# Optimization experiments

Hardware: AMD Instinct MI355X
Metric: run time of the kernel (lower is better)

## Reference

```python
import jax, jax.numpy as jnp
import numpy as np

N_ITEMS = 50000
N_USERS = 20000
N_NODES = N_ITEMS + N_USERS
D = 128
N_REL = 3
NNZ = 800000
K_LAYERS = 2
B, S, L = 256, 4, 50


def setup_inputs() -> dict:
    key = jax.random.key(0)
    ks = iter(jax.random.split(key, 40))
    stdv = float(1.0 / np.sqrt(D))

    def uni(shape):
        return jax.random.uniform(next(ks), shape, jnp.float32, -stdv, stdv)

    id_emb = (jax.random.normal(next(ks), (N_ITEMS, D), jnp.float32) * 0.1).at[0].set(0.0)  # padding_idx=0
    user_emb = jax.random.normal(next(ks), (N_USERS, D), jnp.float32) * 0.1
    inp = dict(
        id_emb=id_emb, user_emb=user_emb,
        lin_r_w=uni((K_LAYERS, N_REL, D, D)),
        upi_w=uni((K_LAYERS, D, D)), upi_b=uni((K_LAYERS, D)),
        upu_w=uni((K_LAYERS, D, D)), upu_b=uni((K_LAYERS, D)),
        w_ih=uni((3 * D, 2 * D)), w_hh=uni((3 * D, D)),
        b_ih=uni((3 * D,)), b_hh=uni((3 * D,)),
        b_iah=uni((D,)), b_oah=uni((D,)),
        ei_w=uni((D, D)), ei_b=uni((D,)),
        eo_w=uni((D, D)), eo_b=uni((D,)),
        q1_w=uni((D, D)), q2_w=uni((D, D)), att_w=uni((D,)),
        fuse_w=uni((D, 2 * D)), fuse_b=uni((D,)),
    )
    # global heterogeneous graph: COO per relation over item+user nodes
    inp['rel_rows'] = jax.random.randint(next(ks), (N_REL, NNZ), 0, N_NODES, dtype=jnp.int32)
    inp['rel_cols'] = jax.random.randint(next(ks), (N_REL, NNZ), 0, N_NODES, dtype=jnp.int32)
    inp['rel_vals'] = jax.random.uniform(next(ks), (N_REL, NNZ), jnp.float32) * 0.1
    # session batch: every session has length in [2, L]
    lens = jax.random.randint(next(ks), (B, S), 2, L + 1)
    raw = jax.random.randint(next(ks), (B, S, L), 1, N_ITEMS)
    inp['ids'] = (raw * (jnp.arange(L)[None, None, :] < lens[:, :, None])).astype(jnp.int32)
    inp['uid'] = jax.random.randint(next(ks), (B,), 0, N_USERS, dtype=jnp.int32)
    inp['u_type'] = jax.random.randint(next(ks), (B,), 0, 3).astype(jnp.float32)
    return inp


def _hgnn(h_item, h_user, rel_rows, rel_cols, rel_vals, lin_r_w, upi_w, upi_b, upu_w, upu_b):
    Ni = h_item.shape[0]
    N = Ni + h_user.shape[0]
    for k in range(lin_r_w.shape[0]):
        h_all = jnp.concatenate([h_item, h_user], 0)
        msg = jnp.zeros_like(h_all)
        for r in range(rel_rows.shape[0]):
            Wh = h_all @ lin_r_w[k, r].T  # per-relation linear
            msg = msg + jax.ops.segment_sum(Wh[rel_cols[r]] * rel_vals[r][:, None],
                                            rel_rows[r], num_segments=N)  # sparse.mm
        h_item = jax.nn.relu((msg[:Ni] + h_item) @ upi_w[k].T + upi_b[k])
        h_user = jax.nn.relu((msg[Ni:] + h_user) @ upu_w[k].T + upu_b[k])
    return h_item, h_user


def reference(id_emb, user_emb, lin_r_w, upi_w, upi_b, upu_w, upu_b,
              w_ih, w_hh, b_ih, b_hh, b_iah, b_oah,
              ei_w, ei_b, eo_w, eo_b, q1_w, q2_w, att_w, fuse_w, fuse_b,
              rel_rows, rel_cols, rel_vals, ids, uid, u_type):
    Bb, Ss, Ll = ids.shape
    N = Ss * Bb
    ids_sb = jnp.transpose(ids, (1, 0, 2)).reshape(N, Ll)  # session-major, matches torch concat order
    lens = (ids_sb != 0).sum(-1)  # >= 2 by construction -> all sessions valid
    rows = jnp.arange(N)
    target = ids_sb[rows, lens - 1]
    Lp = Ll - 1
    m_in = jnp.arange(Lp)[None, :] < (lens - 1)[:, None]
    seq_in = ids_sb[:, :Lp] * m_in
    # session graph: consecutive-item edges; in-half sub-diagonal, out-half super-diagonal
    valid = (m_in[:, 1:] & m_in[:, :-1]).astype(jnp.float32)  # [N, Lp-1]
    i1 = jnp.arange(1, Lp)
    i0 = jnp.arange(Lp - 1)
    a_in = jnp.zeros((N, Lp, Lp), jnp.float32).at[:, i1, i0].set(valid)
    a_out = jnp.zeros((N, Lp, Lp), jnp.float32).at[:, i0, i1].set(valid)
    deg = jnp.clip(a_in.sum(-1), 1.0, None)[..., None]
    a_in = a_in / deg
    a_out = a_out / deg
    h = id_emb[seq_in]  # [N, Lp, D]
    # SessionGNN GRU-style cell (step=1)
    m_i = jnp.matmul(a_in, h @ ei_w.T + ei_b) + b_iah
    m_o = jnp.matmul(a_out, h @ eo_w.T + eo_b) + b_oah
    gi = jnp.concatenate([m_i, m_o], -1) @ w_ih.T + b_ih
    gh = h @ w_hh.T + b_hh
    i_r, i_i, i_n = jnp.split(gi, 3, -1)
    h_r, h_i, h_n = jnp.split(gh, 3, -1)
    rg = jax.nn.sigmoid(i_r + h_r)
    zg = jax.nn.sigmoid(i_i + h_i)
    ng = jnp.tanh(i_n + rg * h_n)
    h = ng + zg * (h - ng)
    # attention readout
    ht = h[rows, jnp.clip(lens - 2, 0, None)]
    alpha = jax.nn.sigmoid((ht @ q1_w.T)[:, None, :] + h @ q2_w.T) @ att_w  # [N, Lp]
    alpha = alpha * m_in.astype(jnp.float32)
    alpha = alpha / (alpha.sum(1, keepdims=True) + 1e-8)
    c_cur = jnp.einsum('nl,nld->nd', alpha, h)
    # global HGNN user context
    g_item, g_user = _hgnn(id_emb[:N_ITEMS], user_emb[:N_USERS], rel_rows, rel_cols,
                           rel_vals, lin_r_w, upi_w, upi_b, upu_w, upu_b)
    c_hist = g_user[jnp.tile(uid, Ss)]
    reps = jnp.concatenate([c_cur, c_hist], -1) @ fuse_w.T + fuse_b
    return reps, target, jnp.tile(u_type, Ss)
```

## Files before the change

kernel.cpp:

```cpp
#include <hip/hip_runtime.h>
#include <hip/hip_bf16.h>

typedef __hip_bfloat16 bf16;
typedef unsigned int uint32;
typedef __attribute__((ext_vector_type(8))) short short8;
typedef __attribute__((ext_vector_type(4))) float f32x4;
typedef __attribute__((ext_vector_type(2))) float f32x2;
typedef __attribute__((ext_vector_type(4))) uint32 u32x4;

#define N_ITEMS_C 50000
#define N_USERS_C 20000
#define N_NODES_C 70000
#define NNZ_C 800000
#define NSESS 1024
#define LP 49
#define NTOK (NSESS * LP)
#define NBK 137

__device__ __forceinline__ float bflo(uint32 u) { return __uint_as_float(u << 16); }
__device__ __forceinline__ float bfhi(uint32 u) { return __uint_as_float(u & 0xffff0000u); }
__device__ __forceinline__ float bfhi_fast(uint32 u) { return __uint_as_float(u); }
__device__ __forceinline__ uint32 packbf(float a, float b) {
    return (uint32)__bfloat16_as_ushort(__float2bfloat16(a)) |
           ((uint32)__bfloat16_as_ushort(__float2bfloat16(b)) << 16);
}

__global__ void init_hab_kernel(const float2* __restrict__ idp, const float2* __restrict__ usp,
                                uint32* __restrict__ hab) {
    int i = blockIdx.x * 256 + threadIdx.x;
    float2 w = (i < 3200000) ? idp[i] : usp[i - 3200000];
    hab[i] = packbf(w.x, w.y);
}

__global__ __launch_bounds__(256) void bucket_hist_kernel(
    const int* __restrict__ rel_rows, int* __restrict__ bhist)
{
    __shared__ int hist[NBK];
    const int r = blockIdx.y, tid = threadIdx.x;
    if (tid < NBK) hist[tid] = 0;
    __syncthreads();
    const int* rr = rel_rows + (size_t)r * NNZ_C;
#pragma unroll
    for (int i = 0; i < 16; ++i) {
        int e = blockIdx.x * 4096 + i * 256 + tid;
        if (e < NNZ_C) atomicAdd(&hist[rr[e] >> 9], 1);
    }
    __syncthreads();
    if (tid < NBK && hist[tid]) atomicAdd(&bhist[r * NBK + tid], hist[tid]);
}

__global__ __launch_bounds__(256) void bucket_scan_kernel(
    const int* __restrict__ bhist, int* __restrict__ bbase)
{
    __shared__ int s[256];
    const int tid = threadIdx.x;
    for (int r = 0; r < 3; ++r) {
        s[tid] = (tid < NBK) ? bhist[r * NBK + tid] : 0;
        __syncthreads();
        for (int d = 1; d < 256; d <<= 1) {
            int t = (tid >= d) ? s[tid - d] : 0;
            __syncthreads();
            s[tid] += t;
            __syncthreads();
        }
        if (tid < NBK) bbase[r * (NBK + 1) + tid + 1] = s[tid];
        if (tid == 0) bbase[r * (NBK + 1)] = 0;
        __syncthreads();
    }
}

__global__ __launch_bounds__(256) void bucket_scatter_kernel(
    const int* __restrict__ rel_rows, const int* __restrict__ rel_cols,
    const float* __restrict__ rel_vals, const int* __restrict__ bbase,
    int* __restrict__ cursor, int2* __restrict__ tmp)
{
    __shared__ int hist[NBK], gbase[NBK], cur2[NBK];
    const int r = blockIdx.y, tid = threadIdx.x;
    if (tid < NBK) { hist[tid] = 0; cur2[tid] = 0; }
    __syncthreads();
    const int* rr = rel_rows + (size_t)r * NNZ_C;
    const int* rc = rel_cols + (size_t)r * NNZ_C;
    const float* rv = rel_vals + (size_t)r * NNZ_C;
#pragma unroll
    for (int i = 0; i < 16; ++i) {
        int e = blockIdx.x * 4096 + i * 256 + tid;
        if (e < NNZ_C) atomicAdd(&hist[rr[e] >> 9], 1);
    }
    __syncthreads();
    if (tid < NBK)
        gbase[tid] = bbase[r * (NBK + 1) + tid] +
                     (hist[tid] ? atomicAdd(&cursor[r * NBK + tid], hist[tid]) : 0);
    __syncthreads();
    int2* tp = tmp + (size_t)r * NNZ_C;
#pragma unroll
    for (int i = 0; i < 16; ++i) {
        int e = blockIdx.x * 4096 + i * 256 + tid;
        if (e < NNZ_C) {
            int row = rr[e];
            int bk = row >> 9;
            int rank = atomicAdd(&cur2[bk], 1);
            uint32 fb = __float_as_uint(rv[e]);
            uint32 pk = (uint32)rc[e] | (((fb >> 16) & 0x7FFFu) << 17);
            tp[gbase[bk] + rank] = make_int2((int)pk, row);
        }
    }
}

__global__ __launch_bounds__(256) void bucket_refine_kernel(
    const int2* __restrict__ tmp, const int* __restrict__ bbase,
    int* __restrict__ offs, uint32* __restrict__ edges)
{
    __shared__ int cnt[512], offsL[512], cur[512];
    __shared__ uint32 outb[6656];
    const int b = blockIdx.x, r = blockIdx.y, tid = threadIdx.x;
    const int lane = tid & 63, wid = tid >> 6;
    const int row0 = b << 9;
    const int e0 = bbase[r * (NBK + 1) + b];
    const int e1 = bbase[r * (NBK + 1) + b + 1];
    cnt[tid] = 0; cnt[256 + tid] = 0; cur[tid] = 0; cur[256 + tid] = 0;
    __syncthreads();
    const int2* tp = tmp + (size_t)r * NNZ_C;
    for (int e = e0 + tid; e < e1; e += 256)
        atomicAdd(&cnt[tp[e].y - row0], 1);
    __syncthreads();
    if (wid == 0) {
        int carry = 0;
        for (int c = 0; c < 8; ++c) {
            int x = cnt[c * 64 + lane];
            int inc = x;
#pragma unroll
            for (int d = 1; d < 64; d <<= 1) {
                int y = __shfl_up(inc, d, 64);
                if (lane >= d) inc += y;
            }
            offsL[c * 64 + lane] = inc - x + carry;
            carry += __shfl(inc, 63, 64);
        }
    }
    __syncthreads();
    for (int i = tid; i < 512; i += 256) {
        int row = row0 + i;
        if (row < 70001) offs[(size_t)r * 70001 + row] = e0 + offsL[i];
    }
    for (int e = e0 + tid; e < e1; e += 256) {
        int2 E = tp[e];
        int lr_ = E.y - row0;
        int slot = offsL[lr_] + atomicAdd(&cur[lr_], 1);
        if (slot < 6656) outb[slot] = (uint32)E.x;
    }
    __syncthreads();
    uint32* eo = edges + (size_t)r * NNZ_C + e0;
    for (int i = tid; i < e1 - e0; i += 256) eo[i] = outb[i];
}

__global__ __launch_bounds__(256) void gather_kernel(
    const uint32* __restrict__ hab, const uint32* __restrict__ edges,
    const int* __restrict__ offs, uint32* __restrict__ T)
{
    const int row = blockIdx.x * 4 + (threadIdx.x >> 6);
    const int lane = threadIdx.x & 63;
    const int grp = lane >> 4;
    const int ql  = lane & 15;
    const char* __restrict__ habB = (const char*)hab + ql * 16;
    f32x2 acc[3][4];
#pragma unroll
    for (int r = 0; r < 3; ++r)
#pragma unroll
        for (int j = 0; j < 4; ++j) acc[r][j] = (f32x2){0.f, 0.f};
#pragma unroll
    for (int r = 0; r < 3; ++r) {
        const uint32* __restrict__ ed = edges + (size_t)r * NNZ_C;
        const int* __restrict__ of = offs + (size_t)r * 70001;
        const int e0 = of[row], e1 = of[row + 1];
        if (e0 >= e1) continue;
        const uint32 span = (uint32)(e1 - e0);
        const int s0 = e0 & ~3;
        for (int eb = s0; eb < e1; eb += 16) {
            const int base = eb + grp * 4;
            uint4 E4 = *(const uint4*)&ed[base];
            uint32 Ej0 = ((uint32)(base + 0 - e0) < span) ? E4.x : 0u;
            uint32 Ej1 = ((uint32)(base + 1 - e0) < span) ? E4.y : 0u;
            uint32 Ej2 = ((uint32)(base + 2 - e0) < span) ? E4.z : 0u;
            uint32 Ej3 = ((uint32)(base + 3 - e0) < span) ? E4.w : 0u;
            uint4 u0 = *(const uint4*)(habB + ((Ej0 & 0x1FFFFu) << 8));
            uint4 u1 = *(const uint4*)(habB + ((Ej1 & 0x1FFFFu) << 8));
            uint4 u2 = *(const uint4*)(habB + ((Ej2 & 0x1FFFFu) << 8));
            uint4 u3 = *(const uint4*)(habB + ((Ej3 & 0x1FFFFu) << 8));
            float v0 = __uint_as_float((Ej0 >> 1) & 0x7FFF0000u);
            float v1 = __uint_as_float((Ej1 >> 1) & 0x7FFF0000u);
            float v2 = __uint_as_float((Ej2 >> 1) & 0x7FFF0000u);
            float v3 = __uint_as_float((Ej3 >> 1) & 0x7FFF0000u);
            f32x2 vv;
            vv = (f32x2){v0, v0};
            acc[r][0] += vv * (f32x2){bflo(u0.x), bfhi_fast(u0.x)};
            acc[r][1] += vv * (f32x2){bflo(u0.y), bfhi_fast(u0.y)};
            acc[r][2] += vv * (f32x2){bflo(u0.z), bfhi_fast(u0.z)};
            acc[r][3] += vv * (f32x2){bflo(u0.w), bfhi_fast(u0.w)};
            vv = (f32x2){v1, v1};
            acc[r][0] += vv * (f32x2){bflo(u1.x), bfhi_fast(u1.x)};
            acc[r][1] += vv * (f32x2){bflo(u1.y), bfhi_fast(u1.y)};
            acc[r][2] += vv * (f32x2){bflo(u1.z), bfhi_fast(u1.z)};
            acc[r][3] += vv * (f32x2){bflo(u1.w), bfhi_fast(u1.w)};
            vv = (f32x2){v2, v2};
            acc[r][0] += vv * (f32x2){bflo(u2.x), bfhi_fast(u2.x)};
            acc[r][1] += vv * (f32x2){bflo(u2.y), bfhi_fast(u2.y)};
            acc[r][2] += vv * (f32x2){bflo(u2.z), bfhi_fast(u2.z)};
            acc[r][3] += vv * (f32x2){bflo(u2.w), bfhi_fast(u2.w)};
            vv = (f32x2){v3, v3};
            acc[r][0] += vv * (f32x2){bflo(u3.x), bfhi_fast(u3.x)};
            acc[r][1] += vv * (f32x2){bflo(u3.y), bfhi_fast(u3.y)};
            acc[r][2] += vv * (f32x2){bflo(u3.z), bfhi_fast(u3.z)};
            acc[r][3] += vv * (f32x2){bflo(u3.w), bfhi_fast(u3.w)};
        }
    }
    float* af = (float*)acc;
#pragma unroll
    for (int off = 16; off < 64; off <<= 1)
#pragma unroll
        for (int j = 0; j < 24; ++j) af[j] += __shfl_xor(af[j], off, 64);
    if (grp == 0) {
#pragma unroll
        for (int r = 0; r < 3; ++r) {
            u32x4 o;
            o.x = packbf(acc[r][0].x, acc[r][0].y);
            o.y = packbf(acc[r][1].x, acc[r][1].y);
            o.z = packbf(acc[r][2].x, acc[r][2].y);
            o.w = packbf(acc[r][3].x, acc[r][3].y);
            __builtin_nontemporal_store(o, (u32x4*)&T[(size_t)row * 192 + r * 64 + ql * 4]);
        }
    }
}

__global__ __launch_bounds__(256, 3) void wprep_kernel(
    const float* __restrict__ upi_w, const float* __restrict__ upu_w,
    const float* __restrict__ lin_r_w, int k, uint32* __restrict__ Wcat)
{
    __shared__ float As[128][65];
    __shared__ __align__(8) bf16 Ws[128][66];
    const int which = blockIdx.y, seg = which / 3, r = which % 3;
    const float* U  = (seg == 0 ? upi_w : upu_w) + (size_t)k * 16384;
    const float* Wr = lin_r_w + (size_t)(k * 3 + r) * 16384;
    uint32* out = Wcat + (size_t)seg * 32768;
    const int tid = threadIdx.x;
    const int row0 = blockIdx.x * 64;
#pragma unroll
    for (int i = 0; i < 8; ++i) {
        int id = i * 256 + tid;
        int rr = id >> 5, c4 = (id & 31) << 2;
        float4 v = *(const float4*)&U[(size_t)(row0 + rr) * 128 + c4];
        As[c4][rr] = v.x; As[c4+1][rr] = v.y; As[c4+2][rr] = v.z; As[c4+3][rr] = v.w;
    }
    const int m0 = (tid & 15) * 4;
    const int n0 = (tid >> 4) * 8;
    float acc[4][8];
#pragma unroll
    for (int i = 0; i < 4; ++i)
#pragma unroll
        for (int j = 0; j < 8; ++j) acc[i][j] = 0.f;
    for (int p = 0; p < 2; ++p) {
        if (p) __syncthreads();
        for (int i = 0; i < 32; ++i) {
            int id = i * 256 + tid;
            int c = id >> 6, kf = id & 63;
            Ws[c][kf] = __float2bfloat16(Wr[(size_t)(p * 64 + kf) * 128 + c]);
        }
        __syncthreads();
        for (int k2 = 0; k2 < 32; ++k2) {
            int kk = p * 64 + 2 * k2;
            float av0[4], av1[4];
#pragma unroll
            for (int i = 0; i < 4; ++i) { av0[i] = As[kk][m0 + i]; av1[i] = As[kk + 1][m0 + i]; }
#pragma unroll
            for (int j = 0; j < 8; ++j) {
                uint32 wp = *(const uint32*)&Ws[n0 + j][2 * k2];
                float w0 = bflo(wp), w1 = bfhi(wp);
#pragma unroll
                for (int i = 0; i < 4; ++i)
                    acc[i][j] = fmaf(av1[i], w1, fmaf(av0[i], w0, acc[i][j]));
            }
        }
    }
#pragma unroll
    for (int i = 0; i < 4; ++i) {
        int n = row0 + m0 + i;
#pragma unroll
        for (int j = 0; j < 8; j += 2)
            out[(size_t)n * 256 + (r * 128 + n0 + j) / 2] = packbf(acc[i][j], acc[i][j + 1]);
    }
}

__global__ __launch_bounds__(256) void upack_kernel(
    const float* __restrict__ upi_w, const float* __restrict__ upu_w,
    int k, uint32* __restrict__ Wcat)
{
    int id = blockIdx.x * 256 + threadIdx.x;
    int seg = id >> 13, p = id & 8191;
    int n = p >> 6, j2 = (p & 63);
    const float* U = (seg ? upu_w : upi_w) + (size_t)k * 16384;
    float2 w = *(const float2*)&U[(size_t)n * 128 + j2 * 2];
    Wcat[(size_t)seg * 32768 + (size_t)n * 256 + 192 + j2] = packbf(w.x, w.y);
}

#define HGNN_ITEM_BLOCKS 391
__global__ __launch_bounds__(256) void hgnn_update_mfma_kernel(
    const bf16* __restrict__ T, uint32* __restrict__ hab,
    const bf16* __restrict__ Wcat, const float* __restrict__ upi_b,
    const float* __restrict__ upu_b, int k)
{
    const int tid = threadIdx.x;
    const int wv = tid >> 6, lane = tid & 63, quad = lane >> 4, lr = lane & 15;
    const int bid = blockIdx.x;
    const int seg = (bid >= HGNN_ITEM_BLOCKS) ? 1 : 0;
    const int row0 = seg ? N_ITEMS_C : 0;
    const int M = seg ? N_USERS_C : N_ITEMS_C;
    const int rbase = (seg ? bid - HGNN_ITEM_BLOCKS : bid) * 128;
    const bf16* __restrict__ Wc = Wcat + (size_t)seg * 65536;
    const float* __restrict__ bias = (seg ? upu_b : upi_b) + k * 128;
    const bf16* hb = (const bf16*)hab;
    f32x4 acc[8][2];
#pragma unroll
    for (int mt = 0; mt < 8; ++mt) { acc[mt][0] = (f32x4){0,0,0,0}; acc[mt][1] = (f32x4){0,0,0,0}; }
    int arow[8];
#pragma unroll
    for (int mt = 0; mt < 8; ++mt) {
        int rr = rbase + mt * 16 + lr;
        arow[mt] = row0 + (rr < M ? rr : M - 1);
    }
#pragma unroll
    for (int ks = 0; ks < 16; ++ks) {
        short8 b0 = *(const short8*)&Wc[(size_t)(wv * 32 + lr) * 512 + ks * 32 + quad * 8];
        short8 b1 = *(const short8*)&Wc[(size_t)(wv * 32 + 16 + lr) * 512 + ks * 32 + quad * 8];
#pragma unroll
        for (int mt = 0; mt < 8; ++mt) {
            short8 a;
            if (ks < 12) a = *(const short8*)&T[(size_t)arow[mt] * 384 + ks * 32 + quad * 8];
            else         a = *(const short8*)&hb[(size_t)arow[mt] * 128 + (ks - 12) * 32 + quad * 8];
            acc[mt][0] = __builtin_amdgcn_mfma_f32_16x16x32_bf16(a, b0, acc[mt][0], 0, 0, 0);
            acc[mt][1] = __builtin_amdgcn_mfma_f32_16x16x32_bf16(a, b1, acc[mt][1], 0, 0, 0);
        }
    }
    __syncthreads();
    unsigned short* hw = (unsigned short*)hab;
#pragma unroll
    for (int s = 0; s < 2; ++s) {
        int col = wv * 32 + s * 16 + lr;
        float bv = bias[col];
#pragma unroll
        for (int mt = 0; mt < 8; ++mt)
#pragma unroll
            for (int reg = 0; reg < 4; ++reg) {
                int rr = rbase + mt * 16 + quad * 4 + reg;
                if (rr < M) {
                    float v = fmaxf(acc[mt][s][reg] + bv, 0.f);
                    hw[(size_t)(row0 + rr) * 128 + col] = __bfloat16_as_ushort(__float2bfloat16(v));
                }
            }
    }
}

__global__ __launch_bounds__(256) void mfma_nt_kernel(
    const bf16* __restrict__ A, const int* __restrict__ rowmap,
    const bf16* __restrict__ W0, const float* __restrict__ b0,
    float* __restrict__ O0, int M)
{
    const int tid = threadIdx.x;
    const int wv = tid >> 6, lane = tid & 63, quad = lane >> 4, lr = lane & 15;
    const int rbase = blockIdx.x * 128;
    int arow[8];
#pragma unroll
    for (int mt = 0; mt < 8; ++mt) {
        int rr = rbase + mt * 16 + lr;
        rr = rr < M ? rr : M - 1;
        arow[mt] = rowmap ? rowmap[rr] : rr;
    }
    f32x4 acc0[8][2];
#pragma unroll
    for (int mt = 0; mt < 8; ++mt) { acc0[mt][0] = (f32x4){0,0,0,0}; acc0[mt][1] = (f32x4){0,0,0,0}; }
#pragma unroll
    for (int ks = 0; ks < 4; ++ks) {
        short8 b00 = *(const short8*)&W0[(size_t)(wv * 32 + lr) * 128 + ks * 32 + quad * 8];
        short8 b01 = *(const short8*)&W0[(size_t)(wv * 32 + 16 + lr) * 128 + ks * 32 + quad * 8];
#pragma unroll
        for (int mt = 0; mt < 8; ++mt) {
            short8 a = *(const short8*)&A[(size_t)arow[mt] * 128 + ks * 32 + quad * 8];
            acc0[mt][0] = __builtin_amdgcn_mfma_f32_16x16x32_bf16(a, b00, acc0[mt][0], 0, 0, 0);
            acc0[mt][1] = __builtin_amdgcn_mfma_f32_16x16x32_bf16(a, b01, acc0[mt][1], 0, 0, 0);
        }
    }
#pragma unroll
    for (int s = 0; s < 2; ++s) {
        int col = wv * 32 + s * 16 + lr;
        float bv0 = b0 ? b0[col] : 0.f;
#pragma unroll
        for (int mt = 0; mt < 8; ++mt)
#pragma unroll
            for (int reg = 0; reg < 4; ++reg) {
                int rr = rbase + mt * 16 + quad * 4 + reg;
                if (rr < M) O0[(size_t)rr * 128 + col] = acc0[mt][s][reg] + bv0;
            }
    }
}

__global__ __launch_bounds__(256) void mfma_agi_kernel(
    const bf16* __restrict__ A,
    const bf16* __restrict__ Wi, const bf16* __restrict__ Wo,
    const float* __restrict__ ei_b, const float* __restrict__ eo_b,
    const float* __restrict__ b_iah, const float* __restrict__ b_oah,
    const int* __restrict__ lens, unsigned short* __restrict__ AgiG)
{
    const int tid = threadIdx.x;
    const int wv = tid >> 6, lane = tid & 63, quad = lane >> 4, lr = lane & 15;
    const int rbase = blockIdx.x * 64;
    int arow[4];
#pragma unroll
    for (int mt = 0; mt < 4; ++mt) arow[mt] = rbase + mt * 16 + lr;
    f32x4 acc0[4][2], acc1[4][2];
#pragma unroll
    for (int mt = 0; mt < 4; ++mt) {
        acc0[mt][0] = (f32x4){0,0,0,0}; acc0[mt][1] = (f32x4){0,0,0,0};
        acc1[mt][0] = (f32x4){0,0,0,0}; acc1[mt][1] = (f32x4){0,0,0,0};
    }
#pragma unroll
    for (int ks = 0; ks < 4; ++ks) {
        short8 b00 = *(const short8*)&Wi[(size_t)(wv * 32 + lr) * 128 + ks * 32 + quad * 8];
        short8 b01 = *(const short8*)&Wi[(size_t)(wv * 32 + 16 + lr) * 128 + ks * 32 + quad * 8];
        short8 b10 = *(const short8*)&Wo[(size_t)(wv * 32 + lr) * 128 + ks * 32 + quad * 8];
        short8 b11 = *(const short8*)&Wo[(size_t)(wv * 32 + 16 + lr) * 128 + ks * 32 + quad * 8];
#pragma unroll
        for (int mt = 0; mt < 4; ++mt) {
            short8 a = *(const short8*)&A[(size_t)arow[mt] * 128 + ks * 32 + quad * 8];
            acc0[mt][0] = __builtin_amdgcn_mfma_f32_16x16x32_bf16(a, b00, acc0[mt][0], 0, 0, 0);
            acc0[mt][1] = __builtin_amdgcn_mfma_f32_16x16x32_bf16(a, b01, acc0[mt][1], 0, 0, 0);
            acc1[mt][0] = __builtin_amdgcn_mfma_f32_16x16x32_bf16(a, b10, acc1[mt][0], 0, 0, 0);
            acc1[mt][1] = __builtin_amdgcn_mfma_f32_16x16x32_bf16(a, b11, acc1[mt][1], 0, 0, 0);
        }
    }
#pragma unroll
    for (int s = 0; s < 2; ++s) {
        int col = wv * 32 + s * 16 + lr;
        float bei = ei_b[col], beo = eo_b[col];
        float bia = b_iah[col], boa = b_oah[col];
#pragma unroll
        for (int mt = 0; mt < 4; ++mt)
#pragma unroll
            for (int reg = 0; reg < 4; ++reg) {
                int rr = rbase + mt * 16 + quad * 4 + reg;
                int d1 = rr + 1; if (d1 == NTOK) d1 = 0;
                int n1 = d1 / LP, t1 = d1 - n1 * LP, l1 = lens[n1];
                float v1 = bia + ((t1 >= 1 && t1 < l1 - 1) ? acc0[mt][s][reg] + bei : 0.f);
                AgiG[(size_t)d1 * 256 + col] = __bfloat16_as_ushort(__float2bfloat16(v1));
                int d2 = rr - 1; if (d2 < 0) d2 = NTOK - 1;
                int n2 = d2 / LP, t2 = d2 - n2 * LP, l2 = lens[n2];
                float v2 = boa + ((t2 < l2 - 2) ? acc1[mt][s][reg] + beo : 0.f);
                AgiG[(size_t)d2 * 256 + 128 + col] = __bfloat16_as_ushort(__float2bfloat16(v2));
            }
    }
}

__global__ void session_prep_kernel(const int* __restrict__ ids, const int* __restrict__ uid,
                                    const float* __restrict__ u_type,
                                    int* __restrict__ lens, int* __restrict__ rowmap,
                                    float* __restrict__ out_target, float* __restrict__ out_utype)
{
    int n = blockIdx.x * 256 + threadIdx.x;
    if (n >= NSESS) return;
    int b = n & 255, s = n >> 8;
    const int* row = ids + (size_t)(b * 4 + s) * 50;
    int len = 0;
#pragma unroll
    for (int l = 0; l < 50; ++l) len += (row[l] != 0) ? 1 : 0;
    lens[n] = len;
    rowmap[n] = n * LP + (len - 2);
    out_target[n] = (float)row[len - 1];
    out_utype[n] = u_type[b];
}

__global__ void chist_kernel(const uint32* __restrict__ hab, const int* __restrict__ uid,
                             float* __restrict__ chist) {
    int n = blockIdx.x, d = threadIdx.x;
    uint32 u = hab[(size_t)(N_ITEMS_C + uid[n & 255]) * 64 + (d >> 1)];
    chist[(size_t)n * 128 + d] = (d & 1) ? bfhi(u) : bflo(u);
}

__global__ void h0_gather_kernel(const float* __restrict__ id_emb, const int* __restrict__ ids,
                                 const int* __restrict__ lens, uint32* __restrict__ hb) {
    int g = blockIdx.x, d = threadIdx.x;
    int n = g / LP;
    int tt = g - n * LP;
    int len = lens[n];
    int b = n & 255, s = n >> 8;
    int id = (tt < len - 1) ? ids[(size_t)(b * 4 + s) * 50 + tt] : 0;
    float2 e = *(const float2*)&id_emb[(size_t)id * 128 + d * 2];
    hb[(size_t)g * 64 + d] = packbf(e.x, e.y);
}

__global__ __launch_bounds__(256) void epack_kernel(
    const float* __restrict__ w_ih, const float* __restrict__ w_hh,
    const float* __restrict__ ei_w, const float* __restrict__ eo_w,
    const float* __restrict__ q2_w, const float* __restrict__ q1_w,
    const float* __restrict__ fuse_w, uint32* __restrict__ dst)
{
    int id = blockIdx.x * 256 + threadIdx.x;
    if (id >= 106496) {
        if (id >= 139264) return;
        int f = id - 106496;
        int kk = f >> 7, n = f & 127;
        ((float*)dst)[id] = fuse_w[(size_t)n * 256 + kk];
        return;
    }
    const float* src; int off;
    if      (id <  49152) { src = w_ih; off = id; }
    else if (id <  73728) { src = w_hh; off = id - 49152; }
    else if (id <  81920) { src = ei_w; off = id - 73728; }
    else if (id <  90112) { src = eo_w; off = id - 81920; }
    else if (id <  98304) { src = q2_w; off = id - 90112; }
    else                  { src = q1_w; off = id - 98304; }
    float2 w = *(const float2*)&src[(size_t)off * 2];
    dst[id] = packbf(w.x, w.y);
}

__global__ __launch_bounds__(256, 2) void gru_mfma_kernel(
    const bf16* __restrict__ Agi,
    uint32* __restrict__ hb,
    const bf16* __restrict__ wihb,
    const bf16* __restrict__ whhb,
    const float* __restrict__ b_ih, const float* __restrict__ b_hh)
{
    const int tid = threadIdx.x;
    const int wv = tid >> 6;
    const int lane = tid & 63;
    const int quad = lane >> 4;
    const int lr = lane & 15;
    const int c0 = wv * 32;
    const int g0 = blockIdx.x * 64;
    int arow[4];
#pragma unroll
    for (int mt = 0; mt < 4; ++mt) arow[mt] = g0 + mt * 16 + lr;

    f32x4 acc[4][2][4];
#pragma unroll
    for (int mt = 0; mt < 4; ++mt)
#pragma unroll
        for (int s = 0; s < 2; ++s)
#pragma unroll
            for (int j = 0; j < 4; ++j) acc[mt][s][j] = (f32x4){0.f, 0.f, 0.f, 0.f};

#pragma unroll 2
    for (int ks = 0; ks < 8; ++ks) {
        short8 bfr[2][3];
#pragma unroll
        for (int s = 0; s < 2; ++s)
#pragma unroll
            for (int gte = 0; gte < 3; ++gte) {
                int n0 = gte * 128 + c0 + s * 16 + lr;
                bfr[s][gte] = *(const short8*)&wihb[(size_t)n0 * 256 + ks * 32 + quad * 8];
            }
#pragma unroll
        for (int mt = 0; mt < 4; ++mt) {
            short8 a = *(const short8*)&Agi[(size_t)arow[mt] * 256 + ks * 32 + quad * 8];
#pragma unroll
            for (int s = 0; s < 2; ++s) {
                acc[mt][s][0] = __builtin_amdgcn_mfma_f32_16x16x32_bf16(a, bfr[s][0], acc[mt][s][0], 0, 0, 0);
                acc[mt][s][1] = __builtin_amdgcn_mfma_f32_16x16x32_bf16(a, bfr[s][1], acc[mt][s][1], 0, 0, 0);
                acc[mt][s][2] = __builtin_amdgcn_mfma_f32_16x16x32_bf16(a, bfr[s][2], acc[mt][s][2], 0, 0, 0);
            }
        }
    }
    const bf16* hbb = (const bf16*)hb;
#pragma unroll 2
    for (int ks = 0; ks < 4; ++ks) {
        short8 bfr[2][3];
#pragma unroll
        for (int s = 0; s < 2; ++s)
#pragma unroll
            for (int gte = 0; gte < 3; ++gte) {
                int n0 = gte * 128 + c0 + s * 16 + lr;
                bfr[s][gte] = *(const short8*)&whhb[(size_t)n0 * 128 + ks * 32 + quad * 8];
            }
#pragma unroll
        for (int mt = 0; mt < 4; ++mt) {
            short8 a = *(const short8*)&hbb[(size_t)arow[mt] * 128 + ks * 32 + quad * 8];
#pragma unroll
            for (int s = 0; s < 2; ++s) {
                acc[mt][s][0] = __builtin_amdgcn_mfma_f32_16x16x32_bf16(a, bfr[s][0], acc[mt][s][0], 0, 0, 0);
                acc[mt][s][1] = __builtin_amdgcn_mfma_f32_16x16x32_bf16(a, bfr[s][1], acc[mt][s][1], 0, 0, 0);
                acc[mt][s][3] = __builtin_amdgcn_mfma_f32_16x16x32_bf16(a, bfr[s][2], acc[mt][s][3], 0, 0, 0);
            }
        }
    }

    __syncthreads();
    unsigned short* hu = (unsigned short*)hb;
#pragma unroll
    for (int s = 0; s < 2; ++s) {
        int col = c0 + s * 16 + lr;
        float brz = b_ih[col] + b_hh[col];
        float bzz = b_ih[col + 128] + b_hh[col + 128];
        float bin = b_ih[col + 256];
        float bhn = b_hh[col + 256];
#pragma unroll
        for (int mt = 0; mt < 4; ++mt)
#pragma unroll
            for (int reg = 0; reg < 4; ++reg) {
                int row = g0 + mt * 16 + quad * 4 + reg;
                float rg = 1.f / (1.f + expf(-(acc[mt][s][0][reg] + brz)));
                float zg = 1.f / (1.f + expf(-(acc[mt][s][1][reg] + bzz)));
                float ng = tanhf(acc[mt][s][2][reg] + bin + rg * (acc[mt][s][3][reg] + bhn));
                size_t idx = (size_t)row * 128 + col;
                float ho = __uint_as_float((uint32)hu[idx] << 16);
                hu[idx] = __bfloat16_as_ushort(__float2bfloat16(ng + zg * (ho - ng)));
            }
    }
}

__global__ __launch_bounds__(128) void attn_fuse_kernel(
    const float* __restrict__ q1h, const float* __restrict__ q2h,
    const unsigned short* __restrict__ hu, const float* __restrict__ chist,
    const int* __restrict__ lens, const float* __restrict__ att_w,
    const float* __restrict__ ftwf, const float* __restrict__ fuse_b,
    float* __restrict__ out)
{
    __shared__ float q1s[128], aws[128], al[64], cv[256];
    const int n = blockIdx.x, tid = threadIdx.x;
    q1s[tid] = q1h[(size_t)n * 128 + tid];
    aws[tid] = att_w[tid];
    if (tid < 64) al[tid] = 0.f;
    __syncthreads();
    const int len = lens[n];
    if (tid < len - 1) {
        const float* q2 = &q2h[(size_t)(n * LP + tid) * 128];
        float s = 0.f;
        for (int d = 0; d < 128; ++d) {
            float x = q1s[d] + q2[d];
            s += aws[d] / (1.f + expf(-x));
        }
        al[tid] = s;
    }
    __syncthreads();
    float ssum = 0.f;
    for (int t = 0; t < len - 1; ++t) ssum += al[t];
    float inv = 1.f / (ssum + 1e-8f);
    float c = 0.f;
    for (int t = 0; t < len - 1; ++t) {
        float hv = __uint_as_float((uint32)hu[(size_t)(n * LP + t) * 128 + tid] << 16);
        c += al[t] * inv * hv;
    }
    cv[tid] = c;
    cv[128 + tid] = chist[(size_t)n * 128 + tid];
    __syncthreads();
    float s = fuse_b[tid];
    for (int kk = 0; kk < 256; ++kk)
        s += cv[kk] * ftwf[(size_t)kk * 128 + tid];
    out[(size_t)n * 128 + tid] = s;
}

extern "C" void kernel_launch(void* const* d_in, const int* in_sizes, int n_in,
                              void* d_out, int out_size, void* d_ws, size_t ws_size,
                              hipStream_t stream)
{
    const float* id_emb   = (const float*)d_in[0];
    const float* user_emb = (const float*)d_in[1];
    const float* lin_r_w  = (const float*)d_in[2];
    const float* upi_w    = (const float*)d_in[3];
    const float* upi_b    = (const float*)d_in[4];
    const float* upu_w    = (const float*)d_in[5];
    const float* upu_b    = (const float*)d_in[6];
    const float* w_ih     = (const float*)d_in[7];
    const float* w_hh     = (const float*)d_in[8];
    const float* b_ih     = (const float*)d_in[9];
    const float* b_hh     = (const float*)d_in[10];
    const float* b_iah    = (const float*)d_in[11];
    const float* b_oah    = (const float*)d_in[12];
    const float* ei_w     = (const float*)d_in[13];
    const float* ei_b     = (const float*)d_in[14];
    const float* eo_w     = (const float*)d_in[15];
    const float* eo_b     = (const float*)d_in[16];
    const float* q1_w     = (const float*)d_in[17];
    const float* q2_w     = (const float*)d_in[18];
    const float* att_w    = (const float*)d_in[19];
    const float* fuse_w   = (const float*)d_in[20];
    const float* fuse_b   = (const float*)d_in[21];
    const int*  rel_rows  = (const int*)d_in[22];
    const int*  rel_cols  = (const int*)d_in[23];
    const float* rel_vals = (const float*)d_in[24];
    const int*  ids       = (const int*)d_in[25];
    const int*  uid       = (const int*)d_in[26];
    const float* u_type   = (const float*)d_in[27];
    float* out = (float*)d_out;

    uint32* W32    = (uint32*)d_ws;
    uint32* hab    = W32;
    uint32* T      = W32 + 4480000;
    uint32* edges  = W32 + 17920000;
    int2*   tmp    = (int2*)(W32 + 20320000);
    int*    offs   = (int*)(W32 + 25120000);
    int*    bhist  = (int*)(W32 + 25330004);
    int*    cursor = (int*)(W32 + 25330415);
    int*    bbase  = (int*)(W32 + 25330826);
    uint32* Wcat   = W32 + 25331240;
    float*  q1h    = (float*)(W32 + 25396776);
    float*  chist  = (float*)(W32 + 25527848);
    int*    lens   = (int*)(W32 + 25658920);
    int*    rowmap = (int*)(W32 + 25659944);
    uint32* sess_hb = W32;
    float* q2h      = (float*)(W32 + 4480000);
    unsigned short* AgiG = (unsigned short*)(W32 + 10902528);
    uint32* wpk     = W32 + 17920000;
    uint32* wihb = wpk;
    uint32* whhb = wpk + 49152;
    uint32* eiwb = wpk + 73728;
    uint32* eowb = wpk + 81920;
    uint32* q2wb = wpk + 90112;
    uint32* q1wb = wpk + 98304;
    float*  ftwf = (float*)(wpk + 106496);
    if (ws_size < (size_t)27144192 * 4 + 4096) return;

    init_hab_kernel<<<17500, 256, 0, stream>>>((const float2*)id_emb, (const float2*)user_emb, hab);
    hipMemsetAsync(bhist, 0, (size_t)822 * 4, stream);
    bucket_hist_kernel<<<dim3(196, 3), 256, 0, stream>>>(rel_rows, bhist);
    bucket_scan_kernel<<<1, 256, 0, stream>>>(bhist, bbase);
    bucket_scatter_kernel<<<dim3(196, 3), 256, 0, stream>>>(rel_rows, rel_cols, rel_vals,
                                                            bbase, cursor, tmp);
    bucket_refine_kernel<<<dim3(NBK, 3), 256, 0, stream>>>(tmp, bbase, offs, edges);

    for (int k = 0; k < 2; ++k) {
        wprep_kernel<<<dim3(2, 6), 256, 0, stream>>>(upi_w, upu_w, lin_r_w, k, Wcat);
        upack_kernel<<<64, 256, 0, stream>>>(upi_w, upu_w, k, Wcat);
        gather_kernel<<<17500, 256, 0, stream>>>(hab, edges, offs, T);
        hgnn_update_mfma_kernel<<<548, 256, 0, stream>>>((const bf16*)T, hab,
            (const bf16*)Wcat, upi_b, upu_b, k);
    }

    session_prep_kernel<<<4, 256, 0, stream>>>(ids, uid, u_type, lens, rowmap,
        out + 131072, out + 132096);
    chist_kernel<<<NSESS, 128, 0, stream>>>(hab, uid, chist);
    epack_kernel<<<544, 256, 0, stream>>>(w_ih, w_hh, ei_w, eo_w, q2_w, q1_w, fuse_w, wpk);
    h0_gather_kernel<<<NTOK, 64, 0, stream>>>(id_emb, ids, lens, sess_hb);
    mfma_agi_kernel<<<784, 256, 0, stream>>>((const bf16*)sess_hb,
        (const bf16*)eiwb, (const bf16*)eowb, ei_b, eo_b, b_iah, b_oah, lens, AgiG);
    gru_mfma_kernel<<<784, 256, 0, stream>>>((const bf16*)AgiG, sess_hb,
        (const bf16*)wihb, (const bf16*)whhb, b_ih, b_hh);
    mfma_nt_kernel<<<392, 256, 0, stream>>>((const bf16*)sess_hb, nullptr,
        (const bf16*)q2wb, nullptr, q2h, NTOK);
    mfma_nt_kernel<<<8, 256, 0, stream>>>((const bf16*)sess_hb, rowmap,
        (const bf16*)q1wb, nullptr, q1h, NSESS);
    attn_fuse_kernel<<<NSESS, 128, 0, stream>>>(q1h, q2h, (const unsigned short*)sess_hb,
        chist, lens, att_w, ftwf, fuse_b, out);
}
```

Measured before the change: 753.9 us.

## Split attention scoring into a parallel alpha kernel and widen several small kernels

The attention score computation moves out of attn_fuse into a new alpha_kernel that gives each token one wavefront with a shuffle reduction, replacing the serial per-thread loop over 128 dims. Separately, init_hab now handles float4 per thread, bucket_scatter keeps row indices in registers instead of reloading them, and h0_gather packs four tokens into each 256-thread block. This adds one kernel launch and an alpha buffer in the workspace. A stray self-assignment line was also inserted into the gather loop.

```diff
diff --git a/kernel.cpp b/kernel.cpp
--- a/kernel.cpp
+++ b/kernel.cpp
@@ -25,11 +25,12 @@
            ((uint32)__bfloat16_as_ushort(__float2bfloat16(b)) << 16);
 }
 
-__global__ void init_hab_kernel(const float2* __restrict__ idp, const float2* __restrict__ usp,
+__global__ void init_hab_kernel(const float4* __restrict__ idp, const float4* __restrict__ usp,
                                 uint32* __restrict__ hab) {
     int i = blockIdx.x * 256 + threadIdx.x;
-    float2 w = (i < 3200000) ? idp[i] : usp[i - 3200000];
-    hab[i] = packbf(w.x, w.y);
+    float4 w = (i < 1600000) ? idp[i] : usp[i - 1600000];
+    uint2 o = make_uint2(packbf(w.x, w.y), packbf(w.z, w.w));
+    *(uint2*)&hab[(size_t)i * 2] = o;
 }
 
 __global__ __launch_bounds__(256) void bucket_hist_kernel(
@@ -81,10 +82,12 @@
     const int* rr = rel_rows + (size_t)r * NNZ_C;
     const int* rc = rel_cols + (size_t)r * NNZ_C;
     const float* rv = rel_vals + (size_t)r * NNZ_C;
+    int rows[16];
 #pragma unroll
     for (int i = 0; i < 16; ++i) {
         int e = blockIdx.x * 4096 + i * 256 + tid;
-        if (e < NNZ_C) atomicAdd(&hist[rr[e] >> 9], 1);
+        rows[i] = (e < NNZ_C) ? rr[e] : -1;
+        if (rows[i] >= 0) atomicAdd(&hist[rows[i] >> 9], 1);
     }
     __syncthreads();
     if (tid < NBK)
@@ -95,13 +98,12 @@
 #pragma unroll
     for (int i = 0; i < 16; ++i) {
         int e = blockIdx.x * 4096 + i * 256 + tid;
-        if (e < NNZ_C) {
-            int row = rr[e];
-            int bk = row >> 9;
+        if (rows[i] >= 0) {
+            int bk = rows[i] >> 9;
             int rank = atomicAdd(&cur2[bk], 1);
             uint32 fb = __float_as_uint(rv[e]);
             uint32 pk = (uint32)rc[e] | (((fb >> 16) & 0x7FFFu) << 17);
-            tp[gbase[bk] + rank] = make_int2((int)pk, row);
+            tp[gbase[bk] + rank] = make_int2((int)pk, rows[i]);
         }
     }
 }
@@ -192,6 +194,7 @@
             float v3 = __uint_as_float((Ej3 >> 1) & 0x7FFF0000u);
             f32x2 vv;
             vv = (f32x2){v0, v0};
+            acc[0 + 0] [0] = acc[0][0];
             acc[r][0] += vv * (f32x2){bflo(u0.x), bfhi_fast(u0.x)};
             acc[r][1] += vv * (f32x2){bflo(u0.y), bfhi_fast(u0.y)};
             acc[r][2] += vv * (f32x2){bflo(u0.z), bfhi_fast(u0.z)};
@@ -482,9 +485,11 @@
     chist[(size_t)n * 128 + d] = (d & 1) ? bfhi(u) : bflo(u);
 }
 
-__global__ void h0_gather_kernel(const float* __restrict__ id_emb, const int* __restrict__ ids,
-                                 const int* __restrict__ lens, uint32* __restrict__ hb) {
-    int g = blockIdx.x, d = threadIdx.x;
+__global__ __launch_bounds__(256) void h0_gather_kernel(
+    const float* __restrict__ id_emb, const int* __restrict__ ids,
+    const int* __restrict__ lens, uint32* __restrict__ hb) {
+    int g = blockIdx.x * 4 + (threadIdx.x >> 6);
+    int d = threadIdx.x & 63;
     int n = g / LP;
     int tt = g - n * LP;
     int len = lens[n];
@@ -613,30 +618,35 @@
     }
 }
 
+__global__ __launch_bounds__(256) void alpha_kernel(
+    const float* __restrict__ q1h, const float* __restrict__ q2h,
+    const float* __restrict__ att_w, const int* __restrict__ lens,
+    float* __restrict__ al)
+{
+    int tok = blockIdx.x * 4 + (threadIdx.x >> 6);
+    int lane = threadIdx.x & 63;
+    int n = tok / LP, t = tok - n * LP;
+    int len = lens[n];
+    float2 q2 = *(const float2*)&q2h[(size_t)tok * 128 + lane * 2];
+    float2 q1 = *(const float2*)&q1h[(size_t)n * 128 + lane * 2];
+    float2 aw = *(const float2*)&att_w[lane * 2];
+    float s = aw.x / (1.f + expf(-(q1.x + q2.x))) + aw.y / (1.f + expf(-(q1.y + q2.y)));
+#pragma unroll
+    for (int off = 1; off < 64; off <<= 1) s += __shfl_xor(s, off, 64);
+    if (lane == 0) al[tok] = (t < len - 1) ? s : 0.f;
+}
+
 __global__ __launch_bounds__(128) void attn_fuse_kernel(
-    const float* __restrict__ q1h, const float* __restrict__ q2h,
-    const unsigned short* __restrict__ hu, const float* __restrict__ chist,
-    const int* __restrict__ lens, const float* __restrict__ att_w,
+    const float* __restrict__ alG, const unsigned short* __restrict__ hu,
+    const float* __restrict__ chist, const int* __restrict__ lens,
     const float* __restrict__ ftwf, const float* __restrict__ fuse_b,
     float* __restrict__ out)
 {
-    __shared__ float q1s[128], aws[128], al[64], cv[256];
+    __shared__ float al[64], cv[256];
     const int n = blockIdx.x, tid = threadIdx.x;
-    q1s[tid] = q1h[(size_t)n * 128 + tid];
-    aws[tid] = att_w[tid];
-    if (tid < 64) al[tid] = 0.f;
+    if (tid < 64) al[tid] = (tid < LP) ? alG[(size_t)n * LP + tid] : 0.f;
     __syncthreads();
     const int len = lens[n];
-    if (tid < len - 1) {
-        const float* q2 = &q2h[(size_t)(n * LP + tid) * 128];
-        float s = 0.f;
-        for (int d = 0; d < 128; ++d) {
-            float x = q1s[d] + q2[d];
-            s += aws[d] / (1.f + expf(-x));
-        }
-        al[tid] = s;
-    }
-    __syncthreads();
     float ssum = 0.f;
     for (int t = 0; t < len - 1; ++t) ssum += al[t];
     float inv = 1.f / (ssum + 1e-8f);
@@ -702,6 +712,7 @@
     float*  chist  = (float*)(W32 + 25527848);
     int*    lens   = (int*)(W32 + 25658920);
     int*    rowmap = (int*)(W32 + 25659944);
+    float*  alG    = (float*)(W32 + 25660968);
     uint32* sess_hb = W32;
     float* q2h      = (float*)(W32 + 4480000);
     unsigned short* AgiG = (unsigned short*)(W32 + 10902528);
@@ -715,7 +726,7 @@
     float*  ftwf = (float*)(wpk + 106496);
     if (ws_size < (size_t)27144192 * 4 + 4096) return;
 
-    init_hab_kernel<<<17500, 256, 0, stream>>>((const float2*)id_emb, (const float2*)user_emb, hab);
+    init_hab_kernel<<<8750, 256, 0, stream>>>((const float4*)id_emb, (const float4*)user_emb, hab);
     hipMemsetAsync(bhist, 0, (size_t)822 * 4, stream);
     bucket_hist_kernel<<<dim3(196, 3), 256, 0, stream>>>(rel_rows, bhist);
     bucket_scan_kernel<<<1, 256, 0, stream>>>(bhist, bbase);
@@ -735,7 +746,7 @@
         out + 131072, out + 132096);
     chist_kernel<<<NSESS, 128, 0, stream>>>(hab, uid, chist);
     epack_kernel<<<544, 256, 0, stream>>>(w_ih, w_hh, ei_w, eo_w, q2_w, q1_w, fuse_w, wpk);
-    h0_gather_kernel<<<NTOK, 64, 0, stream>>>(id_emb, ids, lens, sess_hb);
+    h0_gather_kernel<<<NTOK / 4, 256, 0, stream>>>(id_emb, ids, lens, sess_hb);
     mfma_agi_kernel<<<784, 256, 0, stream>>>((const bf16*)sess_hb,
         (const bf16*)eiwb, (const bf16*)eowb, ei_b, eo_b, b_iah, b_oah, lens, AgiG);
     gru_mfma_kernel<<<784, 256, 0, stream>>>((const bf16*)AgiG, sess_hb,
@@ -744,6 +755,7 @@
         (const bf16*)q2wb, nullptr, q2h, NTOK);
     mfma_nt_kernel<<<8, 256, 0, stream>>>((const bf16*)sess_hb, rowmap,
         (const bf16*)q1wb, nullptr, q1h, NSESS);
-    attn_fuse_kernel<<<NSESS, 128, 0, stream>>>(q1h, q2h, (const unsigned short*)sess_hb,
-        chist, lens, att_w, ftwf, fuse_b, out);
-}
+    alpha_kernel<<<NTOK / 4, 256, 0, stream>>>(q1h, q2h, att_w, lens, alG);
+    attn_fuse_kernel<<<NSESS, 128, 0, stream>>>(alG, (const unsigned short*)sess_hb,
+        chist, lens, ftwf, fuse_b, out);
+}
```

Measured after the change: 769.7 us. +2.1%, slower.
